# Kernel tuning notes

Hardware: AMD Instinct MI355X
Metric: run time of the kernel (lower is better)

The kernel has to match this reference:

```python
import jax, jax.numpy as jnp
import numpy as np

B, T, H, V = 64, 512, 300, 50257


def setup_inputs() -> dict:
    key = jax.random.key(0)
    k0, k1, k2, k3, k4 = jax.random.split(key, 5)
    tokens = jax.random.randint(k0, (B, T), 0, V, dtype=jnp.int32)
    ihs = jnp.zeros((B, H), jnp.float32)
    emb = jax.random.normal(k1, (V, H), jnp.float32) * 0.02
    W = jax.random.normal(k2, (H, H), jnp.float32) * (1.0 / np.sqrt(H))
    U = jax.random.normal(k3, (H, H), jnp.float32) * (1.0 / np.sqrt(H))
    Wout = jax.random.normal(k4, (V, H), jnp.float32) * 0.02
    bout = jnp.zeros((V,), jnp.float32)
    return {"ihs": ihs, "tokens": tokens, "emb": emb, "W": W, "U": U,
            "Wout": Wout, "bout": bout}


def reference(ihs, tokens, emb, W, U, Wout, bout):
    # Embedding lookup: [B, T, H]
    x = emb[tokens]
    # Precompute input projection for all timesteps: U x_t (Linear: x @ U^T)
    ux = jnp.einsum('bth,gh->btg', x, U)  # [B, T, H]
    ux_tmajor = jnp.swapaxes(ux, 0, 1)    # [T, B, H]

    def step(h, ux_t):
        # h_t = tanh(W h_{t-1} + U x_t)
        h_next = jnp.tanh(h @ W.T + ux_t)
        return h_next, h_next

    h_last, _ = jax.lax.scan(step, ihs, ux_tmajor)
    # final hidden state -> vocab logits
    logits = h_last @ Wout.T + bout  # [B, V]
    return logits
```

## Files before the change

kernel.cpp:

```cpp
#include <hip/hip_runtime.h>
#include <math.h>

#define H 300
#define BB 64
#define TT 512
#define VV 50257
#define KC 30

__global__ void transpose_k(const float* __restrict__ in, float* __restrict__ out) {
    int idx = blockIdx.x * blockDim.x + threadIdx.x;
    if (idx < H * H) {
        int r = idx / H, c = idx - r * H;
        out[idx] = in[c * H + r];
    }
}

__global__ __launch_bounds__(256) void ux_k(const int* __restrict__ tokens,
                                            const float* __restrict__ emb,
                                            const float* __restrict__ Ut,
                                            float* __restrict__ ux) {
    __shared__ __align__(16) float x_s[KC][BB];
    __shared__ __align__(16) float ut_s[KC][304];
    __shared__ int tok_s[BB];

    const int t = blockIdx.x;
    const int tid = threadIdx.x;
    if (tid < BB) tok_s[tid] = tokens[tid * TT + t];

    const int tb = tid >> 4;
    const int tg = tid & 15;
    const int b0 = tb * 4;
    const int g0 = tg * 20;
    const bool active = (tg < 15);

    float acc[4][20];
#pragma unroll
    for (int i = 0; i < 4; ++i)
#pragma unroll
        for (int j = 0; j < 20; ++j) acc[i][j] = 0.f;

    __syncthreads();

    for (int h0 = 0; h0 < H; h0 += KC) {
        for (int i = tid; i < BB * 32; i += 256) {
            int b = i >> 5, k = i & 31;
            if (k < KC) x_s[k][b] = emb[tok_s[b] * H + h0 + k];
        }
        for (int i = tid; i < KC * H; i += 256) {
            int k = i / H, g = i - k * H;
            ut_s[k][g] = Ut[(h0 + k) * H + g];
        }
        __syncthreads();
        if (active) {
#pragma unroll 2
            for (int k = 0; k < KC; ++k) {
                float4 xa = *reinterpret_cast<const float4*>(&x_s[k][b0]);
                float4 u0 = *reinterpret_cast<const float4*>(&ut_s[k][g0 + 0]);
                float4 u1 = *reinterpret_cast<const float4*>(&ut_s[k][g0 + 4]);
                float4 u2 = *reinterpret_cast<const float4*>(&ut_s[k][g0 + 8]);
                float4 u3 = *reinterpret_cast<const float4*>(&ut_s[k][g0 + 12]);
                float4 u4 = *reinterpret_cast<const float4*>(&ut_s[k][g0 + 16]);
                const float xr[4] = {xa.x, xa.y, xa.z, xa.w};
                const float ur[20] = {u0.x, u0.y, u0.z, u0.w,
                                      u1.x, u1.y, u1.z, u1.w,
                                      u2.x, u2.y, u2.z, u2.w,
                                      u3.x, u3.y, u3.z, u3.w,
                                      u4.x, u4.y, u4.z, u4.w};
#pragma unroll
                for (int i = 0; i < 4; ++i)
#pragma unroll
                    for (int j = 0; j < 20; ++j)
                        acc[i][j] += xr[i] * ur[j];
            }
        }
        __syncthreads();
    }

    if (active) {
#pragma unroll
        for (int i = 0; i < 4; ++i) {
            float* dst = ux + (t * BB + b0 + i) * H + g0;
#pragma unroll
            for (int jq = 0; jq < 5; ++jq) {
                *reinterpret_cast<float4*>(dst + jq * 4) =
                    make_float4(acc[i][jq * 4 + 0], acc[i][jq * 4 + 1],
                                acc[i][jq * 4 + 2], acc[i][jq * 4 + 3]);
            }
        }
    }
}

#define RNN_Q15(X) X(0) X(1) X(2) X(3) X(4) X(5) X(6) X(7) X(8) X(9) \
    X(10) X(11) X(12) X(13) X(14)

__device__ __forceinline__ void rnn_bar_lds() {
    __builtin_amdgcn_sched_barrier(0);
    asm volatile("s_waitcnt lgkmcnt(0)" ::: "memory");
    __builtin_amdgcn_s_barrier();
    __builtin_amdgcn_sched_barrier(0);
}

__global__ __attribute__((amdgpu_flat_work_group_size(768, 768), amdgpu_waves_per_eu(3, 3)))
void rnn_k(const float* __restrict__ W,
           const float* __restrict__ ux,
           const float* __restrict__ ihs,
           float* __restrict__ hlast) {
    __shared__ __align__(16) float shpool[20800];
    float* h_s = shpool;
    float* p_s = shpool + 304;

    const int b = blockIdx.x;
    const int tid = threadIdx.x;
    const int tt = (tid < 750) ? tid : 749;
    const int c  = tt / 150;
    const int g2 = tt - c * 150;

    const float4* w0p = reinterpret_cast<const float4*>(W + (size_t)(g2      ) * H + c * 60);
    const float4* w1p = reinterpret_cast<const float4*>(W + (size_t)(g2 + 150) * H + c * 60);

#define RNN_DW(q) float4 w0_##q = w0p[q]; float4 w1_##q = w1p[q];
    RNN_Q15(RNN_DW)
#undef RNN_DW

    if (tid < H) h_s[tid] = ihs[b * H + tid];

    const float* uxr = ux + (size_t)b * H + tid;
    float u = 0.f;
    if (tid < H) u = uxr[0];
    __syncthreads();

    const float4* hs4 = reinterpret_cast<const float4*>(h_s);
    const int c15 = c * 15;

#pragma unroll 1
    for (int t = 0; t < TT; ++t) {
        float n = 0.f;
        if (tid < H && t + 1 < TT)
            n = uxr[(size_t)(t + 1) * (BB * H)];
        float4 a0 = make_float4(0.f, 0.f, 0.f, 0.f);
        float4 a1 = make_float4(0.f, 0.f, 0.f, 0.f);
#define RNN_FMA(q) { float4 h4 = hs4[c15 + q]; \
        a0.x += w0_##q.x * h4.x; a0.y += w0_##q.y * h4.y; \
        a0.z += w0_##q.z * h4.z; a0.w += w0_##q.w * h4.w; \
        a1.x += w1_##q.x * h4.x; a1.y += w1_##q.y * h4.y; \
        a1.z += w1_##q.z * h4.z; a1.w += w1_##q.w * h4.w; }
        RNN_Q15(RNN_FMA)
#undef RNN_FMA
        float pA = (a0.x + a0.y) + (a0.z + a0.w);
        float pB = (a1.x + a1.y) + (a1.z + a1.w);
        if (tid < 750) {
            p_s[c * 304 + g2      ] = pA;
            p_s[c * 304 + g2 + 150] = pB;
        }
        rnn_bar_lds();
        if (tid < H) {
            float z = p_s[tid] + u;
            z += p_s[304 + tid];
            z += p_s[608 + tid];
            z += p_s[912 + tid];
            z += p_s[1216 + tid];
            float e = __expf(2.f * z);
            h_s[tid] = 1.f - 2.f * __builtin_amdgcn_rcpf(e + 1.f);
        }
        u = n;
        rnn_bar_lds();
    }
    if (tid < H) hlast[b * H + tid] = h_s[tid];
}

__global__ __launch_bounds__(256) void logits_k(const float* __restrict__ hlast,
                                                const float* __restrict__ Wout,
                                                const float* __restrict__ bout,
                                                float* __restrict__ out) {
    __shared__ __align__(16) float Ws[32 * 132];
    __shared__ __align__(16) float hs[32 * 76];
    const int tid = threadIdx.x;
    const int tv = tid & 31;
    const int tb = tid >> 5;
    const int v0 = blockIdx.x * 128;

    float acc[8][4];
#pragma unroll
    for (int i = 0; i < 8; ++i)
#pragma unroll
        for (int j = 0; j < 4; ++j) acc[i][j] = 0.f;

    for (int hb = 0; hb < H; hb += 32) {
        __syncthreads();
        {
            const int vp = tid >> 1;
            const int hloc = (tid & 1) * 16;
            int vv = v0 + vp; if (vv > VV - 1) vv = VV - 1;
            const float* wrow = Wout + (size_t)vv * H + hb + hloc;
#pragma unroll
            for (int i = 0; i < 4; ++i) {
                const int hg = hb + hloc + i * 4;
                float4 val;
                if (hg + 3 < H) {
                    val = *reinterpret_cast<const float4*>(wrow + i * 4);
                } else {
                    val.x = (hg + 0 < H) ? wrow[i * 4 + 0] : 0.f;
                    val.y = (hg + 1 < H) ? wrow[i * 4 + 1] : 0.f;
                    val.z = (hg + 2 < H) ? wrow[i * 4 + 2] : 0.f;
                    val.w = (hg + 3 < H) ? wrow[i * 4 + 3] : 0.f;
                }
                Ws[(hloc + i * 4 + 0) * 132 + vp] = val.x;
                Ws[(hloc + i * 4 + 1) * 132 + vp] = val.y;
                Ws[(hloc + i * 4 + 2) * 132 + vp] = val.z;
                Ws[(hloc + i * 4 + 3) * 132 + vp] = val.w;
            }
        }
        {
            const int bb = tid >> 2;
            const int hl = (tid & 3) * 8;
            const float* hrow = hlast + bb * H + hb + hl;
#pragma unroll
            for (int i = 0; i < 2; ++i) {
                const int hg = hb + hl + i * 4;
                float4 val;
                if (hg + 3 < H) {
                    val = *reinterpret_cast<const float4*>(hrow + i * 4);
                } else {
                    val.x = (hg + 0 < H) ? hrow[i * 4 + 0] : 0.f;
                    val.y = (hg + 1 < H) ? hrow[i * 4 + 1] : 0.f;
                    val.z = (hg + 2 < H) ? hrow[i * 4 + 2] : 0.f;
                    val.w = (hg + 3 < H) ? hrow[i * 4 + 3] : 0.f;
                }
                hs[(hl + i * 4 + 0) * 76 + bb] = val.x;
                hs[(hl + i * 4 + 1) * 76 + bb] = val.y;
                hs[(hl + i * 4 + 2) * 76 + bb] = val.z;
                hs[(hl + i * 4 + 3) * 76 + bb] = val.w;
            }
        }
        __syncthreads();
        const float4* Ws4 = reinterpret_cast<const float4*>(Ws);
        const float4* hs4 = reinterpret_cast<const float4*>(hs);
#pragma unroll
        for (int h2 = 0; h2 < 32; ++h2) {
            float4 w4  = Ws4[h2 * 33 + tv];
            float4 h4a = hs4[h2 * 19 + tb * 2];
            float4 h4b = hs4[h2 * 19 + tb * 2 + 1];
            const float hv[8] = {h4a.x, h4a.y, h4a.z, h4a.w,
                                 h4b.x, h4b.y, h4b.z, h4b.w};
#pragma unroll
            for (int bi = 0; bi < 8; ++bi) {
                acc[bi][0] += hv[bi] * w4.x;
                acc[bi][1] += hv[bi] * w4.y;
                acc[bi][2] += hv[bi] * w4.z;
                acc[bi][3] += hv[bi] * w4.w;
            }
        }
    }

    const int vg = v0 + tv * 4;
    float4 bq;
    if (vg + 3 < VV) bq = *reinterpret_cast<const float4*>(bout + vg);
    else {
        bq.x = (vg + 0 < VV) ? bout[vg + 0] : 0.f;
        bq.y = (vg + 1 < VV) ? bout[vg + 1] : 0.f;
        bq.z = (vg + 2 < VV) ? bout[vg + 2] : 0.f;
        bq.w = (vg + 3 < VV) ? bout[vg + 3] : 0.f;
    }
#pragma unroll
    for (int bi = 0; bi < 8; ++bi) {
        const int bb = tb * 8 + bi;
        float* op = out + (size_t)bb * VV + vg;
        if (vg + 0 < VV) op[0] = acc[bi][0] + bq.x;
        if (vg + 1 < VV) op[1] = acc[bi][1] + bq.y;
        if (vg + 2 < VV) op[2] = acc[bi][2] + bq.z;
        if (vg + 3 < VV) op[3] = acc[bi][3] + bq.w;
    }
}

extern "C" void kernel_launch(void* const* d_in, const int* in_sizes, int n_in,
                              void* d_out, int out_size, void* d_ws, size_t ws_size,
                              hipStream_t stream) {
    const float* ihs    = (const float*)d_in[0];
    const int*   tokens = (const int*)  d_in[1];
    const float* emb    = (const float*)d_in[2];
    const float* W      = (const float*)d_in[3];
    const float* U      = (const float*)d_in[4];
    const float* Wout   = (const float*)d_in[5];
    const float* bout   = (const float*)d_in[6];
    float* out = (float*)d_out;

    char* ws = (char*)d_ws;
    float* Ut    = (float*)(ws + 0);
    float* hlast = (float*)(ws + 400000);
    float* ux    = (float*)(ws + 1048576);

    const int tp_blocks = (H * H + 255) / 256;
    transpose_k<<<tp_blocks, 256, 0, stream>>>(U, Ut);
    ux_k<<<TT, 256, 0, stream>>>(tokens, emb, Ut, ux);
    rnn_k<<<BB, 768, 0, stream>>>(W, ux, ihs, hlast);
    logits_k<<<(VV + 127) / 128, 256, 0, stream>>>(hlast, Wout, bout, out);
}
```

Before: 726.5 us.

## Shrink RNN block to 512 threads with three output rows per thread

The recurrent kernel now runs 500 active threads (5 column chunks × 100 row groups), and each thread keeps three rows of W in registers instead of two, so the block has 8 waves instead of 12. Empty inline asm statements pin the 180 weight registers inside the loop so the compiler cannot rematerialise or spill them. The custom LDS barrier is replaced with plain __syncthreads. The aim is lower barrier cost per timestep from fewer waves, at the price of more serial FMAs per thread and heavy register pressure.

```diff
diff --git a/kernel.cpp b/kernel.cpp
--- a/kernel.cpp
+++ b/kernel.cpp
@@ -93,14 +93,7 @@
 #define RNN_Q15(X) X(0) X(1) X(2) X(3) X(4) X(5) X(6) X(7) X(8) X(9) \
     X(10) X(11) X(12) X(13) X(14)
 
-__device__ __forceinline__ void rnn_bar_lds() {
-    __builtin_amdgcn_sched_barrier(0);
-    asm volatile("s_waitcnt lgkmcnt(0)" ::: "memory");
-    __builtin_amdgcn_s_barrier();
-    __builtin_amdgcn_sched_barrier(0);
-}
-
-__global__ __attribute__((amdgpu_flat_work_group_size(768, 768), amdgpu_waves_per_eu(3, 3)))
+__global__ __attribute__((amdgpu_flat_work_group_size(512, 512), amdgpu_waves_per_eu(2, 2)))
 void rnn_k(const float* __restrict__ W,
            const float* __restrict__ ux,
            const float* __restrict__ ihs,
@@ -111,14 +104,24 @@
 
     const int b = blockIdx.x;
     const int tid = threadIdx.x;
-    const int tt = (tid < 750) ? tid : 749;
-    const int c  = tt / 150;
-    const int g2 = tt - c * 150;
-
-    const float4* w0p = reinterpret_cast<const float4*>(W + (size_t)(g2      ) * H + c * 60);
-    const float4* w1p = reinterpret_cast<const float4*>(W + (size_t)(g2 + 150) * H + c * 60);
-
-#define RNN_DW(q) float4 w0_##q = w0p[q]; float4 w1_##q = w1p[q];
+    const int tt = (tid < 500) ? tid : 499;
+    const int c  = tt / 100;
+    const int g3 = tt - c * 100;
+
+    const float4* w0p = reinterpret_cast<const float4*>(W + (size_t)(g3      ) * H + c * 60);
+    const float4* w1p = reinterpret_cast<const float4*>(W + (size_t)(g3 + 100) * H + c * 60);
+    const float4* w2p = reinterpret_cast<const float4*>(W + (size_t)(g3 + 200) * H + c * 60);
+
+#define RNN_DW(q) \
+    float4 t0_##q = w0p[q]; \
+    float w0_##q##_x = t0_##q.x, w0_##q##_y = t0_##q.y, \
+          w0_##q##_z = t0_##q.z, w0_##q##_w = t0_##q.w; \
+    float4 t1_##q = w1p[q]; \
+    float w1_##q##_x = t1_##q.x, w1_##q##_y = t1_##q.y, \
+          w1_##q##_z = t1_##q.z, w1_##q##_w = t1_##q.w; \
+    float4 t2_##q = w2p[q]; \
+    float w2_##q##_x = t2_##q.x, w2_##q##_y = t2_##q.y, \
+          w2_##q##_z = t2_##q.z, w2_##q##_w = t2_##q.w;
     RNN_Q15(RNN_DW)
 #undef RNN_DW
 
@@ -132,27 +135,44 @@
     const float4* hs4 = reinterpret_cast<const float4*>(h_s);
     const int c15 = c * 15;
 
+#define PINQ(r, q) "+v"(w##r##_##q##_x), "+v"(w##r##_##q##_y), \
+                   "+v"(w##r##_##q##_z), "+v"(w##r##_##q##_w)
+
 #pragma unroll 1
     for (int t = 0; t < TT; ++t) {
+        asm volatile("" : PINQ(0, 0), PINQ(0, 1), PINQ(0, 2), PINQ(0, 3), PINQ(0, 4));
+        asm volatile("" : PINQ(0, 5), PINQ(0, 6), PINQ(0, 7), PINQ(0, 8), PINQ(0, 9));
+        asm volatile("" : PINQ(0, 10), PINQ(0, 11), PINQ(0, 12), PINQ(0, 13), PINQ(0, 14));
+        asm volatile("" : PINQ(1, 0), PINQ(1, 1), PINQ(1, 2), PINQ(1, 3), PINQ(1, 4));
+        asm volatile("" : PINQ(1, 5), PINQ(1, 6), PINQ(1, 7), PINQ(1, 8), PINQ(1, 9));
+        asm volatile("" : PINQ(1, 10), PINQ(1, 11), PINQ(1, 12), PINQ(1, 13), PINQ(1, 14));
+        asm volatile("" : PINQ(2, 0), PINQ(2, 1), PINQ(2, 2), PINQ(2, 3), PINQ(2, 4));
+        asm volatile("" : PINQ(2, 5), PINQ(2, 6), PINQ(2, 7), PINQ(2, 8), PINQ(2, 9));
+        asm volatile("" : PINQ(2, 10), PINQ(2, 11), PINQ(2, 12), PINQ(2, 13), PINQ(2, 14));
         float n = 0.f;
         if (tid < H && t + 1 < TT)
             n = uxr[(size_t)(t + 1) * (BB * H)];
         float4 a0 = make_float4(0.f, 0.f, 0.f, 0.f);
         float4 a1 = make_float4(0.f, 0.f, 0.f, 0.f);
+        float4 a2 = make_float4(0.f, 0.f, 0.f, 0.f);
 #define RNN_FMA(q) { float4 h4 = hs4[c15 + q]; \
-        a0.x += w0_##q.x * h4.x; a0.y += w0_##q.y * h4.y; \
-        a0.z += w0_##q.z * h4.z; a0.w += w0_##q.w * h4.w; \
-        a1.x += w1_##q.x * h4.x; a1.y += w1_##q.y * h4.y; \
-        a1.z += w1_##q.z * h4.z; a1.w += w1_##q.w * h4.w; }
+        a0.x += w0_##q##_x * h4.x; a0.y += w0_##q##_y * h4.y; \
+        a0.z += w0_##q##_z * h4.z; a0.w += w0_##q##_w * h4.w; \
+        a1.x += w1_##q##_x * h4.x; a1.y += w1_##q##_y * h4.y; \
+        a1.z += w1_##q##_z * h4.z; a1.w += w1_##q##_w * h4.w; \
+        a2.x += w2_##q##_x * h4.x; a2.y += w2_##q##_y * h4.y; \
+        a2.z += w2_##q##_z * h4.z; a2.w += w2_##q##_w * h4.w; }
         RNN_Q15(RNN_FMA)
 #undef RNN_FMA
-        float pA = (a0.x + a0.y) + (a0.z + a0.w);
-        float pB = (a1.x + a1.y) + (a1.z + a1.w);
-        if (tid < 750) {
-            p_s[c * 304 + g2      ] = pA;
-            p_s[c * 304 + g2 + 150] = pB;
-        }
-        rnn_bar_lds();
+        float pA0 = (a0.x + a0.y) + (a0.z + a0.w);
+        float pA1 = (a1.x + a1.y) + (a1.z + a1.w);
+        float pA2 = (a2.x + a2.y) + (a2.z + a2.w);
+        if (tid < 500) {
+            p_s[c * 304 + g3      ] = pA0;
+            p_s[c * 304 + g3 + 100] = pA1;
+            p_s[c * 304 + g3 + 200] = pA2;
+        }
+        __syncthreads();
         if (tid < H) {
             float z = p_s[tid] + u;
             z += p_s[304 + tid];
@@ -163,8 +183,9 @@
             h_s[tid] = 1.f - 2.f * __builtin_amdgcn_rcpf(e + 1.f);
         }
         u = n;
-        rnn_bar_lds();
-    }
+        __syncthreads();
+    }
+#undef PINQ
     if (tid < H) hlast[b * H + tid] = h_s[tid];
 }
 
@@ -292,6 +313,6 @@
     const int tp_blocks = (H * H + 255) / 256;
     transpose_k<<<tp_blocks, 256, 0, stream>>>(U, Ut);
     ux_k<<<TT, 256, 0, stream>>>(tokens, emb, Ut, ux);
-    rnn_k<<<BB, 768, 0, stream>>>(W, ux, ihs, hlast);
+    rnn_k<<<BB, 512, 0, stream>>>(W, ux, ihs, hlast);
     logits_k<<<(VV + 127) / 128, 256, 0, stream>>>(hlast, Wout, bout, out);
 }
```

Result: slower. 812.1 us (+11.8%).
